# Kernel optimization log

Measured on AMD Instinct MI355X. Metric: run time of the kernel, lower is better.

The kernel has to match this reference:

```python
import jax, jax.numpy as jnp
import numpy as np

DIM = 512
L = 4096
B, H, W = 8, 64, 64
EPS = 1e-06
BN_EPS = 1e-05


def setup_inputs() -> dict:
    key = jax.random.key(0)
    ks = jax.random.split(key, 16)
    s = 1.0 / np.sqrt(DIM)
    d = {
        'x': jax.random.normal(ks[0], (B, DIM, H, W), dtype=jnp.float32),
        'pos_emb': jax.random.normal(ks[1], (1, L, DIM), dtype=jnp.float32),
        'Wq': jax.random.uniform(ks[2], (DIM, DIM), jnp.float32, -s, s),
        'bq': jax.random.uniform(ks[3], (DIM,), jnp.float32, -s, s),
        'Wk': jax.random.uniform(ks[4], (DIM, DIM), jnp.float32, -s, s),
        'bk': jax.random.uniform(ks[5], (DIM,), jnp.float32, -s, s),
        'Wv': jax.random.uniform(ks[6], (DIM, DIM), jnp.float32, -s, s),
        'bv': jax.random.uniform(ks[7], (DIM,), jnp.float32, -s, s),
        'Wq1': jax.random.uniform(ks[8], (DIM, DIM), jnp.float32, -s, s),
        'bq1': jax.random.uniform(ks[9], (DIM,), jnp.float32, -s, s),
        'Wk1': jax.random.uniform(ks[10], (DIM, DIM), jnp.float32, -s, s),
        'bk1': jax.random.uniform(ks[11], (DIM,), jnp.float32, -s, s),
        'gamma': jax.random.normal(ks[12], (1,), jnp.float32) * 0.1,
        'bn_weight': jnp.ones((DIM,), jnp.float32),
        'bn_bias': jnp.zeros((DIM,), jnp.float32),
    }
    return d


def reference(x, pos_emb, Wq, bq, Wk, bk, Wv, bv, Wq1, bq1, Wk1, bk1, gamma, bn_weight, bn_bias):
    Bb, C, Hh, Ww = x.shape
    # [B,C,H,W] -> [B, L, C] tokens
    xs = x.transpose(0, 2, 3, 1).reshape(Bb, Hh * Ww, C) + pos_emb
    Q = jax.nn.relu(xs @ Wq.T + bq)   # kernel_fun = ReLU
    K = jax.nn.relu(xs @ Wk.T + bk)
    V = xs @ Wv.T + bv
    Q1 = xs @ Wq1.T + bq1
    K1 = xs @ Wk1.T + bk1
    # torch einsum 'blc,bcc,bl->blc' uses only diag(KV); compute it directly:
    # diagKV[b,c] = sum_l K[b,l,c] * V[b,l,c]
    diagKV = jnp.einsum('blc,blc->bc', K, V)
    Ksum = K.sum(axis=1)  # == K^T summed over last axis, [B,C]
    Z = 1.0 / jnp.einsum('blc,bc->bl', Q, Ksum + EPS)
    result = Q * diagKV[:, None, :] * Z[:, :, None]  # [B,L,C]
    # channel-softmax attention: softmax over last dim of Q1^T @ K1, [B,C,C]
    mid = jax.nn.softmax(jnp.einsum('blc,bld->bcd', Q1, K1), axis=-1)
    result = result @ mid  # [B,L,C]
    xs = xs + gamma * result
    y = xs.transpose(0, 2, 1).reshape(Bb, C, Hh, Ww)
    # BatchNorm2d in training mode (fresh module): batch stats, biased variance
    mean = y.mean(axis=(0, 2, 3))
    var = y.var(axis=(0, 2, 3))
    yn = (y - mean[None, :, None, None]) * jax.lax.rsqrt(var + BN_EPS)[None, :, None, None]
    yn = yn * bn_weight[None, :, None, None] + bn_bias[None, :, None, None]
    return jax.nn.relu(yn)
```

## Files before the change

kernel.cpp:

```cpp
#include <hip/hip_runtime.h>
#include <stdint.h>

typedef float f32x4 __attribute__((ext_vector_type(4)));
typedef short bf16x8 __attribute__((ext_vector_type(8)));

__device__ __forceinline__ float bf2f(unsigned short h){
  union { unsigned int u; float f; } v; v.u = ((unsigned int)h) << 16; return v.f;
}
__device__ __forceinline__ unsigned short f2bf(float f){
  union { float f; unsigned int u; } v; v.f = f;
  return (unsigned short)((v.u + 0x7fffu + ((v.u >> 16) & 1u)) >> 16);
}

typedef __attribute__((address_space(1))) const unsigned int ga_u32;
typedef __attribute__((address_space(3))) unsigned int ls_u32;
__device__ __forceinline__ void async_load16(const void* g, void* l){
  __builtin_amdgcn_global_load_lds((ga_u32*)g, (ls_u32*)l, 16, 0, 0);
}

#define CFENCE() asm volatile("" ::: "memory")

__global__ __launch_bounds__(256) void k_prep_all(
    const float* __restrict__ w0, const float* __restrict__ w1,
    const float* __restrict__ w2, const float* __restrict__ w3,
    const float* __restrict__ w4,
    const float* __restrict__ b0, const float* __restrict__ b1,
    const float* __restrict__ b2, const float* __restrict__ b3,
    const float* __restrict__ b4,
    unsigned short* __restrict__ wbf, float* __restrict__ bias5,
    unsigned short* __restrict__ wq1x2)
{
  const int bid = blockIdx.x;
  const int t = threadIdx.x;
  if (bid < 5120){
    int slot = bid >> 10;
    int i = (bid & 1023) * 256 + t;
    const float* w = (slot == 0) ? w0 : (slot == 1) ? w1 :
                     (slot == 2) ? w2 : (slot == 3) ? w3 : w4;
    wbf[(size_t)slot * 262144 + i] = f2bf(w[i]);
  } else if (bid < 5130){
    int i = (bid - 5120) * 256 + t;
    int s = i >> 9, r = i & 511;
    const float* b = (s == 0) ? b0 : (s == 1) ? b1 : (s == 2) ? b2 :
                     (s == 3) ? b3 : b4;
    bias5[i] = b[r];
  } else {
    int e = bid - 5130;
    #pragma unroll
    for (int rep = 0; rep < 2; rep++){
      int idx = rep*256 + t;
      unsigned short v = f2bf(w3[e*512 + idx]);
      wq1x2[(size_t)e*1024 + idx] = v;
      wq1x2[(size_t)e*1024 + 512 + idx] = v;
    }
  }
}

__global__ __launch_bounds__(256) void k_build_xs(
    const float* __restrict__ x, const float* __restrict__ pos,
    unsigned short* __restrict__ xsb, unsigned short* __restrict__ xsT,
    float* __restrict__ svec)
{
  __shared__ float tile[64][65];
  __shared__ unsigned short tile2[64][72];
  __shared__ float sred[256];
  const int lt = blockIdx.x, ct = blockIdx.y;
  const int t = threadIdx.x;
  const int rr = t >> 3, c8 = (t & 7) * 8;
  float pr[16];
  #pragma unroll
  for (int pass = 0; pass < 2; pass++){
    int gl = lt*64 + rr + pass*32;
    f32x4 p0 = *(const f32x4*)(pos + (size_t)gl * 512 + ct*64 + c8);
    f32x4 p1 = *(const f32x4*)(pos + (size_t)gl * 512 + ct*64 + c8 + 4);
    #pragma unroll
    for (int s = 0; s < 4; s++){ pr[pass*8+s] = p0[s]; pr[pass*8+4+s] = p1[s]; }
  }
  for (int b = 0; b < 8; b++){
    #pragma unroll
    for (int pass = 0; pass < 2; pass++){
      int r = rr + pass * 32;
      const float* src = x + ((size_t)b * 512 + ct*64 + r) * 4096 + lt*64 + c8;
      f32x4 v0 = *(const f32x4*)src;
      f32x4 v1 = *(const f32x4*)(src + 4);
      #pragma unroll
      for (int s = 0; s < 4; s++){ tile[r][c8+s] = v0[s]; tile[r][c8+4+s] = v1[s]; }
    }
    __syncthreads();
    #pragma unroll
    for (int pass = 0; pass < 2; pass++){
      int ll = rr + pass * 32;
      int gl = lt*64 + ll;
      bf16x8 hv;
      #pragma unroll
      for (int s = 0; s < 8; s++){
        unsigned short h = f2bf(tile[c8+s][ll] + pr[pass*8+s]);
        hv[s] = (short)h;
        tile2[c8+s][ll] = h;
      }
      *(bf16x8*)(xsb + ((size_t)b * 4096 + gl) * 512 + ct*64 + c8) = hv;
    }
    __syncthreads();
    #pragma unroll
    for (int rep = 0; rep < 2; rep++){
      int c = rep*32 + (t >> 3);
      int l0 = (t & 7) * 8;
      bf16x8 v = *(const bf16x8*)&tile2[c][l0];
      *(bf16x8*)(xsT + ((size_t)b * 512 + ct*64 + c) * 4096 + lt*64 + l0) = v;
    }
    {
      const int c = t & 63, lq = t >> 6;
      float s_ = 0.f;
      #pragma unroll
      for (int j = 0; j < 16; j++) s_ += bf2f(tile2[c][lq*16 + j]);
      sred[t] = s_;
      __syncthreads();
      if (t < 64){
        float ss = sred[t] + sred[t+64] + sred[t+128] + sred[t+192];
        atomicAdd(&svec[b*512 + ct*64 + t], ss);
      }
    }
    __syncthreads();
  }
}

__global__ __launch_bounds__(64) void k_softmax(
    const float* __restrict__ S, unsigned short* __restrict__ mid)
{
  const size_t row = blockIdx.x;
  const int lane = threadIdx.x;
  const float* p = S + row * 512 + lane * 8;
  f32x4 v0 = *(const f32x4*)p, v1 = *(const f32x4*)(p + 4);
  float mx = v0[0];
  #pragma unroll
  for (int s = 1; s < 4; s++) mx = fmaxf(mx, v0[s]);
  #pragma unroll
  for (int s = 0; s < 4; s++) mx = fmaxf(mx, v1[s]);
  #pragma unroll
  for (int m = 1; m < 64; m <<= 1) mx = fmaxf(mx, __shfl_xor(mx, m));
  float e[8]; float sum = 0.f;
  #pragma unroll
  for (int s = 0; s < 4; s++){ e[s]   = __expf(v0[s] - mx); sum += e[s]; }
  #pragma unroll
  for (int s = 0; s < 4; s++){ e[4+s] = __expf(v1[s] - mx); sum += e[4+s]; }
  #pragma unroll
  for (int m = 1; m < 64; m <<= 1) sum += __shfl_xor(sum, m);
  float inv = 1.0f / sum;
  bf16x8 hv;
  #pragma unroll
  for (int s = 0; s < 8; s++) hv[s] = (short)f2bf(e[s] * inv);
  *(bf16x8*)(mid + row * 512 + lane * 8) = hv;
}

__global__ __launch_bounds__(256) void k_transpose_scale(
    const unsigned short* __restrict__ in, const float* __restrict__ diag,
    unsigned short* __restrict__ out)
{
  __shared__ float tile[64][65];
  const int rt = blockIdx.x, ct = blockIdx.y, z = blockIdx.z;
  const unsigned short* src = in  + (size_t)z * 262144;
  unsigned short*       dst = out + (size_t)z * 262144;
  const int t = threadIdx.x;
  const int rr = t >> 3, c8 = (t & 7) * 8;
  #pragma unroll
  for (int pass = 0; pass < 2; pass++){
    int r = rr + pass * 32;
    bf16x8 v = *(const bf16x8*)(src + (size_t)(rt*64 + r) * 512 + ct*64 + c8);
    #pragma unroll
    for (int s = 0; s < 8; s++) tile[r][c8+s] = bf2f((unsigned short)v[s]);
  }
  __syncthreads();
  f32x4 dg0 = *(const f32x4*)(diag + z*512 + rt*64 + c8);
  f32x4 dg1 = *(const f32x4*)(diag + z*512 + rt*64 + c8 + 4);
  #pragma unroll
  for (int pass = 0; pass < 2; pass++){
    int c = rr + pass * 32;
    bf16x8 hv;
    #pragma unroll
    for (int s = 0; s < 4; s++) hv[s]   = (short)f2bf(tile[c8+s][c]   * dg0[s]);
    #pragma unroll
    for (int s = 0; s < 4; s++) hv[4+s] = (short)f2bf(tile[c8+4+s][c] * dg1[s]);
    *(bf16x8*)(dst + (size_t)(ct*64 + c) * 512 + rt*64 + c8) = hv;
  }
}

#define GEMM_PRE()                                                            \
  const int tid = threadIdx.x;                                                \
  const int lane = tid & 63;                                                  \
  const int wave = tid >> 6;                                                  \
  const int wm = wave >> 1, wn = wave & 1;                                    \
  size_t aoff[4], boff[4]; int ldsq[4];                                       \
  _Pragma("unroll")                                                           \
  for (int i = 0; i < 4; i++){                                                \
    int qq = i*4 + wave;                                                      \
    int ch = qq*64 + lane;                                                    \
    int m  = ch >> 3, p = ch & 7;                                             \
    int lc = p ^ (m & 7);                                                     \
    aoff[i] = (size_t)(m0 + m) * K + lc*8;                                    \
    boff[i] = (size_t)m * K + lc*8;                                           \
    ldsq[i] = qq * 1024;                                                      \
  }                                                                           \
  f32x4 acc[4][4];                                                            \
  const f32x4 vzero = {0.f,0.f,0.f,0.f};                                      \
  _Pragma("unroll")                                                           \
  for (int i = 0; i < 4; i++)                                                 \
    _Pragma("unroll")                                                         \
    for (int j = 0; j < 4; j++) acc[i][j] = vzero;                            \
  int arow[4], brow[4];                                                       \
  _Pragma("unroll")                                                           \
  for (int f = 0; f < 4; f++){                                                \
    arow[f] = (wm*64 + f*16 + (lane & 15)) * 64;                              \
    brow[f] = (wn*64 + f*16 + (lane & 15)) * 64;                              \
  }                                                                           \
  const int kg = lane >> 4;                                                   \
  const int l7 = lane & 7;                                                    \
  const int l15 = lane & 15;

#define GEMM_STAGE2(buf, kt, BB)                                              \
  _Pragma("unroll")                                                           \
  for (int i = 0; i < 4; i++){                                                \
    async_load16(Ae + aoff[i] + (kt)*64, (char*)&smem[(buf)*8192] + ldsq[i]); \
    async_load16((BB) + boff[i] + (kt)*64, (char*)&smem[16384 + (buf)*8192] + ldsq[i]); \
  }

#define GEMM_COMPUTE2(buf, ACC)                                               \
  _Pragma("unroll")                                                           \
  for (int ks = 0; ks < 2; ks++){                                             \
    bf16x8 a[4], b[4];                                                        \
    const int pa = (ks*4 + kg) ^ l7;                                          \
    _Pragma("unroll")                                                         \
    for (int f = 0; f < 4; f++){                                              \
      a[f] = *(const bf16x8*)&smem[(buf)*8192 + arow[f] + pa*8];              \
      b[f] = *(const bf16x8*)&smem[16384 + (buf)*8192 + brow[f] + pa*8];      \
    }                                                                         \
    _Pragma("unroll")                                                         \
    for (int i = 0; i < 4; i++)                                               \
      _Pragma("unroll")                                                       \
      for (int j = 0; j < 4; j++)                                             \
        (ACC)[i][j] = __builtin_amdgcn_mfma_f32_16x16x32_bf16(a[i], b[j], (ACC)[i][j], 0, 0, 0); \
  }

#define GEMM_KLOOP2(nkt, BB)                                                  \
  GEMM_STAGE2(0, 0, BB);                                                      \
  __syncthreads();                                                            \
  { int cur = 0;                                                              \
    for (int kt = 0; kt < (nkt); kt++){                                       \
      if (kt + 1 < (nkt)) { GEMM_STAGE2(cur ^ 1, kt + 1, BB); }               \
      GEMM_COMPUTE2(cur, acc);                                                \
      __syncthreads();                                                        \
      cur ^= 1;                                                               \
    } }

__global__ __launch_bounds__(256, 2) void k_mega(
    const unsigned short* __restrict__ A,
    const unsigned short* __restrict__ xsT,
    const unsigned short* __restrict__ W,
    const float* __restrict__ bias5,
    const float* __restrict__ svec,
    unsigned short* __restrict__ Qb,
    unsigned short* __restrict__ Gstk,
    float* __restrict__ diag, float* __restrict__ ksum,
    float* __restrict__ uvec, float* __restrict__ wvec)
{
  __shared__ unsigned short smem[32768];
  const int bid = blockIdx.x;
  const int xcd = bid & 7, local = bid >> 3;

  if (local < 32){
    const int gw = xcd*32 + local;
    const int part = gw & 1;
    const int ntile = (gw >> 1) & 3;
    const int mtile = (gw >> 3) & 3;
    const int z = gw >> 5;
    const int m0 = mtile * 128, n0 = ntile * 128;
    const int K = 4096;
    const unsigned short* Ae = xsT + (size_t)z * 2097152 + part * 2048;
    const unsigned short* Be = Ae + (size_t)n0 * 4096;

    GEMM_PRE();
    GEMM_KLOOP2(32, Be);

    #pragma unroll
    for (int j = 0; j < 4; j++){
      const int cl = wn*64 + j*16 + l15;
      #pragma unroll
      for (int i = 0; i < 4; i++){
        const int rb = wm*64 + i*16 + kg*4;
        #pragma unroll
        for (int q = 0; q < 4; q++)
          smem[(rb + q)*136 + cl] = f2bf(acc[i][j][q]);
      }
    }
    __syncthreads();
    #pragma unroll
    for (int rep = 0; rep < 8; rep++){
      const int rl = rep*16 + (tid >> 4);
      const int c0 = (tid & 15) * 8;
      bf16x8 v = *(const bf16x8*)&smem[rl*136 + c0];
      *(bf16x8*)(Gstk + (size_t)z*524288 + (size_t)(m0 + rl)*1024 + part*512 + n0 + c0) = v;
    }
    return;
  }

  if (local >= 288){
    const int uwid = xcd*2 + (local - 288);
    const int sel = uwid & 1, b = uwid >> 1;
    const int t = threadIdx.x;
    float* sv = (float*)(void*)smem;
    sv[t] = svec[b*512 + t]; sv[t+256] = svec[b*512 + t + 256];
    __syncthreads();
    const unsigned short* Wp = W + (size_t)(3 + sel) * 262144;
    float* o = sel ? wvec : uvec;
    #pragma unroll
    for (int rep = 0; rep < 2; rep++){
      int e = rep*256 + t;
      const unsigned short* row = Wp + (size_t)e * 512;
      float acc_ = 0.f;
      for (int ch = 0; ch < 64; ch++){
        bf16x8 v = *(const bf16x8*)(row + ch*8);
        #pragma unroll
        for (int j = 0; j < 8; j++) acc_ += bf2f((unsigned short)v[j]) * sv[ch*8+j];
      }
      o[b*512 + e] = acc_;
    }
    return;
  }

  const int pw = xcd*256 + (local - 32);
  const int mtile = pw >> 3;
  const int unit  = pw & 7;
  const int m0 = mtile * 128;
  const int K = 512;
  const unsigned short* Ae = A;

  int mode, cb;
  const unsigned short* BeK; const unsigned short* BeV = W;
  if (unit < 4){ mode = 0; cb = unit*128;     BeK = W + (size_t)cb * 512; }
  else         { mode = 1; cb = (unit-4)*128; BeK = W + 262144 + (size_t)cb * 512;
                                              BeV = W + 524288 + (size_t)cb * 512; }

  GEMM_PRE();

  if (mode == 1){
    const int bz = mtile >> 5;
    GEMM_STAGE2(0, 0, BeK);
    __syncthreads();
    int cur = 0;
    for (int kt = 0; kt < 8; kt++){
      if (kt < 7) { GEMM_STAGE2(cur ^ 1, kt + 1, BeK); }
      else        { GEMM_STAGE2(cur ^ 1, 0, BeV); }
      GEMM_COMPUTE2(cur, acc);
      __syncthreads();
      cur ^= 1;
    }
    GEMM_STAGE2(cur ^ 1, 1, BeV);
    unsigned int kpk[4][4][2];
    #pragma unroll
    for (int j = 0; j < 4; j++){
      const int cj = cb + wn*64 + j*16 + l15;
      const float bb = bias5[512 + cj];
      float ks_ = 0.f;
      #pragma unroll
      for (int i = 0; i < 4; i++){
        #pragma unroll
        for (int h = 0; h < 2; h++){
          float v0 = acc[i][j][2*h]   + bb; v0 = v0 > 0.f ? v0 : 0.f;
          float v1 = acc[i][j][2*h+1] + bb; v1 = v1 > 0.f ? v1 : 0.f;
          unsigned short h0 = f2bf(v0), h1 = f2bf(v1);
          kpk[i][j][h] = (unsigned)h0 | ((unsigned)h1 << 16);
          ks_ += bf2f(h0) + bf2f(h1);
        }
        acc[i][j] = vzero;
      }
      ks_ += __shfl_xor(ks_, 16);
      ks_ += __shfl_xor(ks_, 32);
      if (lane < 16) atomicAdd(&ksum[bz*512 + cj], ks_);
    }
    for (int kt = 0; kt < 8; kt++){
      if (kt >= 1 && kt < 7) { GEMM_STAGE2(cur ^ 1, kt + 1, BeV); }
      GEMM_COMPUTE2(cur, acc);
      __syncthreads();
      cur ^= 1;
    }
    #pragma unroll
    for (int j = 0; j < 4; j++){
      const int cj = cb + wn*64 + j*16 + l15;
      const float bb = bias5[1024 + cj];
      float dv = 0.f;
      #pragma unroll
      for (int i = 0; i < 4; i++){
        #pragma unroll
        for (int h = 0; h < 2; h++){
          float v0 = bf2f(f2bf(acc[i][j][2*h]   + bb));
          float v1 = bf2f(f2bf(acc[i][j][2*h+1] + bb));
          dv += bf2f((unsigned short)(kpk[i][j][h] & 0xffffu)) * v0
              + bf2f((unsigned short)(kpk[i][j][h] >> 16))     * v1;
        }
      }
      dv += __shfl_xor(dv, 16);
      dv += __shfl_xor(dv, 32);
      if (lane < 16) atomicAdd(&diag[bz*512 + cj], dv);
    }
    return;
  }

  GEMM_KLOOP2(8, BeK);

  #pragma unroll
  for (int j = 0; j < 4; j++){
    const int cl = wn*64 + j*16 + l15;
    const float bb = bias5[cb + cl];
    #pragma unroll
    for (int i = 0; i < 4; i++){
      const int rb = wm*64 + i*16 + kg*4;
      #pragma unroll
      for (int q = 0; q < 4; q++){
        float v = acc[i][j][q] + bb; v = v > 0.f ? v : 0.f;
        smem[(rb + q)*136 + cl] = f2bf(v);
      }
    }
  }
  __syncthreads();
  #pragma unroll
  for (int rep = 0; rep < 8; rep++){
    const int rl = rep*16 + (tid >> 4);
    const int c0 = (tid & 15) * 8;
    bf16x8 v = *(const bf16x8*)&smem[rl*136 + c0];
    *(bf16x8*)(Qb + (size_t)(m0 + rl) * 512 + cb + c0) = v;
  }
}

__global__ __launch_bounds__(256) void k_pz(
    const unsigned short* __restrict__ Wq1x2,
    const unsigned short* __restrict__ Gstk,
    unsigned short* __restrict__ P,
    const unsigned short* __restrict__ Qb,
    const float* __restrict__ ksum,
    float* __restrict__ Z)
{
  __shared__ unsigned short smem[32768];
  const int bid = blockIdx.x;

  if (bid >= 128){
    const int row = (bid - 128) * 4 + ((int)threadIdx.x >> 6);
    const int lane = threadIdx.x & 63;
    const int b = row >> 12;
    bf16x8 q = *(const bf16x8*)(Qb + (size_t)row * 512 + lane * 8);
    f32x4 k0 = *(const f32x4*)(ksum + b*512 + lane*8);
    f32x4 k1 = *(const f32x4*)(ksum + b*512 + lane*8 + 4);
    float den = 0.f;
    #pragma unroll
    for (int s = 0; s < 4; s++) den += bf2f((unsigned short)q[s])   * (k0[s] + 1e-6f);
    #pragma unroll
    for (int s = 0; s < 4; s++) den += bf2f((unsigned short)q[4+s]) * (k1[s] + 1e-6f);
    #pragma unroll
    for (int m = 1; m < 64; m <<= 1) den += __shfl_xor(den, m);
    if (lane == 0) Z[row] = 1.0f / den;
    return;
  }

  const int wgid = (bid & 7) * 16 + (bid >> 3);
  const int z = wgid >> 4;
  const int mtile = (wgid >> 2) & 3, ntile = wgid & 3;
  const int m0 = mtile * 128, n0 = ntile * 128;
  const int K = 1024;
  const unsigned short* Ae = Wq1x2;
  const unsigned short* Be = Gstk + (size_t)z * 524288 + (size_t)n0 * 1024;

  GEMM_PRE();
  GEMM_KLOOP2(16, Be);

  #pragma unroll
  for (int j = 0; j < 4; j++){
    const int cl = wn*64 + j*16 + l15;
    #pragma unroll
    for (int i = 0; i < 4; i++){
      const int rb = wm*64 + i*16 + kg*4;
      #pragma unroll
      for (int q = 0; q < 4; q++)
        smem[(rb + q)*136 + cl] = f2bf(acc[i][j][q]);
    }
  }
  __syncthreads();
  #pragma unroll
  for (int rep = 0; rep < 8; rep++){
    const int rl = rep*16 + (tid >> 4);
    const int c0 = (tid & 15) * 8;
    bf16x8 v = *(const bf16x8*)&smem[rl*136 + c0];
    *(bf16x8*)(P + (size_t)z * 262144 + (size_t)(m0 + rl) * 512 + n0 + c0) = v;
  }
}

__global__ __launch_bounds__(256) void gemm_S(
    const unsigned short* __restrict__ P,
    const unsigned short* __restrict__ Wk1b,
    const float* __restrict__ bias5,
    const float* __restrict__ u, const float* __restrict__ w,
    float* __restrict__ Sf)
{
  __shared__ unsigned short smem[32768];
  const int bid = blockIdx.x;
  const int wgid = (bid & 7) * 16 + (bid >> 3);
  const int z = wgid >> 4;
  const int mtile = (wgid >> 2) & 3, ntile = wgid & 3;
  const int m0 = mtile * 128, n0 = ntile * 128;
  const int K = 512;
  const unsigned short* Ae = P + (size_t)z * 262144;
  const unsigned short* Be = Wk1b + (size_t)n0 * 512;

  GEMM_PRE();
  GEMM_KLOOP2(8, Be);

  #pragma unroll
  for (int j = 0; j < 4; j++){
    int cd = n0 + wn*64 + j*16 + l15;
    float bkv = bias5[2048 + cd];
    float wv  = w[z*512 + cd] + 4096.0f * bkv;
    #pragma unroll
    for (int i = 0; i < 4; i++){
      int r = m0 + wm*64 + i*16 + kg*4;
      #pragma unroll
      for (int q = 0; q < 4; q++){
        int rr = r + q;
        float uq  = u[z*512 + rr];
        float bqv = bias5[1536 + rr];
        Sf[(size_t)z * 262144 + (size_t)rr * 512 + cd] =
            acc[i][j][q] + uq * bkv + bqv * wv;
      }
    }
  }
}

__global__ __launch_bounds__(256, 2) void gemm_res2(
    const unsigned short* __restrict__ A,
    const unsigned short* __restrict__ Bt,
    const float* __restrict__ Zp,
    unsigned short* __restrict__ outh,
    const float* __restrict__ gamma_p,
    float* __restrict__ bnS, float* __restrict__ bnQ)
{
  __shared__ unsigned short smem[32768];
  __shared__ float zbuf[128];
  const int bid = blockIdx.x;
  const int wgid = (bid & 7) * 128 + (bid >> 3);
  const int mtile = wgid >> 2;
  const int ntile = wgid & 3;
  const int m0 = mtile * 128;
  const int nc0 = ntile * 128;
  const int K = 512;
  const unsigned short* Ae = A;
  const unsigned short* Be =
      Bt + (size_t)(mtile >> 5) * 262144 + (size_t)nc0 * 512;

  GEMM_PRE();
  GEMM_KLOOP2(8, Be);

  const float g = gamma_p[0];
  if (tid < 128) zbuf[tid] = Zp[m0 + tid];
  __syncthreads();
  #pragma unroll
  for (int j = 0; j < 4; j++){
    const int cl = wn*64 + j*16 + l15;
    #pragma unroll
    for (int i = 0; i < 4; i++){
      const int rb = wm*64 + i*16 + kg*4;
      #pragma unroll
      for (int q = 0; q < 4; q++){
        const int rl = rb + q;
        smem[rl*136 + cl] = f2bf(g * zbuf[rl] * acc[i][j][q]);
      }
    }
  }
  __syncthreads();
  float sc[8] = {0.f,0.f,0.f,0.f,0.f,0.f,0.f,0.f};
  float sq[8] = {0.f,0.f,0.f,0.f,0.f,0.f,0.f,0.f};
  const int c0 = (tid & 15) * 8;
  #pragma unroll
  for (int rep = 0; rep < 8; rep++){
    const int rl = rep*16 + (tid >> 4);
    bf16x8 ga = *(const bf16x8*)&smem[rl*136 + c0];
    size_t gidx = (size_t)(m0 + rl) * 512 + nc0 + c0;
    bf16x8 xv = *(const bf16x8*)(outh + gidx);
    bf16x8 yv;
    #pragma unroll
    for (int j = 0; j < 8; j++){
      float y = bf2f((unsigned short)xv[j]) + bf2f((unsigned short)ga[j]);
      yv[j] = (short)f2bf(y);
      sc[j] += y; sq[j] += y * y;
    }
    *(bf16x8*)(outh + gidx) = yv;
  }
  __syncthreads();
  float* red = (float*)(void*)smem;
  const int tg = tid >> 4;
  f32x4 s0 = {sc[0],sc[1],sc[2],sc[3]}, s1 = {sc[4],sc[5],sc[6],sc[7]};
  f32x4 q0 = {sq[0],sq[1],sq[2],sq[3]}, q1 = {sq[4],sq[5],sq[6],sq[7]};
  *(f32x4*)&red[tg*128 + c0]        = s0;  *(f32x4*)&red[tg*128 + c0 + 4]        = s1;
  *(f32x4*)&red[2048 + tg*128 + c0] = q0;  *(f32x4*)&red[2048 + tg*128 + c0 + 4] = q1;
  __syncthreads();
  if (tid < 128){
    float ss = 0.f, qq = 0.f;
    #pragma unroll
    for (int gg = 0; gg < 16; gg++){
      ss += red[gg*128 + tid];
      qq += red[2048 + gg*128 + tid];
    }
    atomicAdd(&bnS[nc0 + tid], ss);
    atomicAdd(&bnQ[nc0 + tid], qq);
  }
}

__global__ __launch_bounds__(256) void k_bn_finalize(
    const unsigned short* __restrict__ y, const float* __restrict__ bnS,
    const float* __restrict__ bnQ, const float* __restrict__ bnw,
    const float* __restrict__ bnb, float* __restrict__ out)
{
  __shared__ float tile[64][65];
  __shared__ float scale_s[64], shift_s[64];
  const int lt = blockIdx.x, ct = blockIdx.y, b = blockIdx.z;
  const int t = threadIdx.x;
  if (t < 64){
    int c = ct*64 + t;
    float s = bnS[c], q = bnQ[c];
    float mean = s * (1.0f / 32768.0f);
    float var  = q * (1.0f / 32768.0f) - mean * mean;
    float inv  = rsqrtf(var + 1e-5f);
    float scv  = bnw[c] * inv;
    scale_s[t] = scv;
    shift_s[t] = bnb[c] - mean * scv;
  }
  const int rr = t >> 3, c8 = (t & 7) * 8;
  #pragma unroll
  for (int pass = 0; pass < 2; pass++){
    int l = rr + pass * 32;
    bf16x8 v = *(const bf16x8*)(y + ((size_t)b * 4096 + lt*64 + l) * 512 + ct*64 + c8);
    #pragma unroll
    for (int s = 0; s < 8; s++) tile[l][c8+s] = bf2f((unsigned short)v[s]);
  }
  __syncthreads();
  #pragma unroll
  for (int pass = 0; pass < 2; pass++){
    int c = rr + pass * 32;
    float scv = scale_s[c], sh = shift_s[c];
    f32x4 o0, o1;
    #pragma unroll
    for (int s = 0; s < 4; s++){
      float v = tile[c8+s][c] * scv + sh;     o0[s] = v > 0.f ? v : 0.f;
      float w = tile[c8+4+s][c] * scv + sh;   o1[s] = w > 0.f ? w : 0.f;
    }
    float* dp = out + ((size_t)b * 512 + ct*64 + c) * 4096 + lt*64 + c8;
    *(f32x4*)dp = o0;
    *(f32x4*)(dp + 4) = o1;
  }
}

extern "C" void kernel_launch(void* const* d_in, const int* in_sizes, int n_in,
                              void* d_out, int out_size, void* d_ws, size_t ws_size,
                              hipStream_t stream)
{
  const float* x    = (const float*)d_in[0];
  const float* pos  = (const float*)d_in[1];
  const float* Wq   = (const float*)d_in[2];
  const float* bq   = (const float*)d_in[3];
  const float* Wk   = (const float*)d_in[4];
  const float* bk   = (const float*)d_in[5];
  const float* Wv   = (const float*)d_in[6];
  const float* bv   = (const float*)d_in[7];
  const float* Wq1  = (const float*)d_in[8];
  const float* bq1  = (const float*)d_in[9];
  const float* Wk1  = (const float*)d_in[10];
  const float* bk1  = (const float*)d_in[11];
  const float* gam  = (const float*)d_in[12];
  const float* bnw  = (const float*)d_in[13];
  const float* bnb  = (const float*)d_in[14];
  float* out = (float*)d_out;
  char* ws = (char*)d_ws;

  const size_t MB = 1ull << 20;
  const size_t OFF_XSB  = 0;
  const size_t OFF_QB   = 32*MB;
  const size_t OFF_XST  = 64*MB;
  const size_t OFF_GSTK = 96*MB;
  const size_t OFF_PBF  = 104*MB;
  const size_t OFF_SF   = 108*MB;
  const size_t OFF_MIDB = 116*MB;
  const size_t OFF_MIDT = 120*MB;
  const size_t OFF_WBF  = 124*MB;
  const size_t OFF_WQ2  = 127*MB;
  const size_t OFF_B5   = 128*MB + 512*1024;
  const size_t OFF_UV   = 129*MB;
  const size_t OFF_WV   = OFF_UV + 16384;
  const size_t OFF_Z    = OFF_WV + 16384;
  const size_t OFF_DIAG = 130*MB;
  const size_t OFF_KSUM = OFF_DIAG + 16384;
  const size_t OFF_BNS  = OFF_KSUM + 16384;
  const size_t OFF_BNQ  = OFF_BNS + 2048;
  const size_t OFF_SV   = OFF_BNQ + 2048;
  const size_t ZERO_LEN = 16384 + 16384 + 2048 + 2048 + 16384;
  const size_t WS_NEED  = OFF_SV + 16384;
  if (ws_size < WS_NEED) return;

  unsigned short* xsb  = (unsigned short*)(ws + OFF_XSB);
  unsigned short* Qb   = (unsigned short*)(ws + OFF_QB);
  unsigned short* xsT  = (unsigned short*)(ws + OFF_XST);
  unsigned short* Gstk = (unsigned short*)(ws + OFF_GSTK);
  unsigned short* Pbf  = (unsigned short*)(ws + OFF_PBF);
  float*          Sf   = (float*)(ws + OFF_SF);
  unsigned short* midb = (unsigned short*)(ws + OFF_MIDB);
  unsigned short* midT = (unsigned short*)(ws + OFF_MIDT);
  unsigned short* wbf  = (unsigned short*)(ws + OFF_WBF);
  unsigned short* wq1x2= (unsigned short*)(ws + OFF_WQ2);
  float* bias5 = (float*)(ws + OFF_B5);
  float* uvec = (float*)(ws + OFF_UV);
  float* wvec = (float*)(ws + OFF_WV);
  float* Zp   = (float*)(ws + OFF_Z);
  float* diag = (float*)(ws + OFF_DIAG);
  float* ksum = (float*)(ws + OFF_KSUM);
  float* bnS  = (float*)(ws + OFF_BNS);
  float* bnQ  = (float*)(ws + OFF_BNQ);
  float* svec = (float*)(ws + OFF_SV);

  hipMemsetAsync(ws + OFF_DIAG, 0, ZERO_LEN, stream);

  k_prep_all<<<dim3(5642), 256, 0, stream>>>(Wq, Wk, Wv, Wq1, Wk1,
                                             bq, bk, bv, bq1, bk1,
                                             wbf, bias5, wq1x2);

  k_build_xs<<<dim3(64, 8), 256, 0, stream>>>(x, pos, xsb, xsT, svec);

  k_mega<<<dim3(2320), 256, 0, stream>>>(xsb, xsT, wbf, bias5, svec,
                                         Qb, Gstk, diag, ksum, uvec, wvec);

  k_pz<<<dim3(8320), 256, 0, stream>>>(wq1x2, Gstk, Pbf, Qb, ksum, Zp);

  gemm_S<<<dim3(128), 256, 0, stream>>>(Pbf, wbf + 4*262144, bias5, uvec, wvec, Sf);

  k_softmax<<<dim3(4096), 64, 0, stream>>>(Sf, midb);
  k_transpose_scale<<<dim3(8, 8, 8), 256, 0, stream>>>(midb, diag, midT);

  gemm_res2<<<dim3(1024), 256, 0, stream>>>(Qb, midT, Zp, xsb, gam, bnS, bnQ);

  k_bn_finalize<<<dim3(64, 8, 8), 256, 0, stream>>>(xsb, bnS, bnQ, bnw, bnb, out);
}
```

Before: 220.4 us.

## Merge weight prep with xs build and fuse softmax with scaled transpose

Result: faster. 215.6 us (-2.2%).

```diff
diff --git a/kernel.cpp b/kernel.cpp
--- a/kernel.cpp
+++ b/kernel.cpp
@@ -20,52 +20,53 @@
 
 #define CFENCE() asm volatile("" ::: "memory")
 
-__global__ __launch_bounds__(256) void k_prep_all(
+__global__ __launch_bounds__(256) void k_prep_build(
+    const float* __restrict__ x, const float* __restrict__ pos,
     const float* __restrict__ w0, const float* __restrict__ w1,
     const float* __restrict__ w2, const float* __restrict__ w3,
     const float* __restrict__ w4,
     const float* __restrict__ b0, const float* __restrict__ b1,
     const float* __restrict__ b2, const float* __restrict__ b3,
     const float* __restrict__ b4,
+    unsigned short* __restrict__ xsb, unsigned short* __restrict__ xsT,
+    float* __restrict__ svec,
     unsigned short* __restrict__ wbf, float* __restrict__ bias5,
     unsigned short* __restrict__ wq1x2)
-{
-  const int bid = blockIdx.x;
-  const int t = threadIdx.x;
-  if (bid < 5120){
-    int slot = bid >> 10;
-    int i = (bid & 1023) * 256 + t;
-    const float* w = (slot == 0) ? w0 : (slot == 1) ? w1 :
-                     (slot == 2) ? w2 : (slot == 3) ? w3 : w4;
-    wbf[(size_t)slot * 262144 + i] = f2bf(w[i]);
-  } else if (bid < 5130){
-    int i = (bid - 5120) * 256 + t;
-    int s = i >> 9, r = i & 511;
-    const float* b = (s == 0) ? b0 : (s == 1) ? b1 : (s == 2) ? b2 :
-                     (s == 3) ? b3 : b4;
-    bias5[i] = b[r];
-  } else {
-    int e = bid - 5130;
-    #pragma unroll
-    for (int rep = 0; rep < 2; rep++){
-      int idx = rep*256 + t;
-      unsigned short v = f2bf(w3[e*512 + idx]);
-      wq1x2[(size_t)e*1024 + idx] = v;
-      wq1x2[(size_t)e*1024 + 512 + idx] = v;
-    }
-  }
-}
-
-__global__ __launch_bounds__(256) void k_build_xs(
-    const float* __restrict__ x, const float* __restrict__ pos,
-    unsigned short* __restrict__ xsb, unsigned short* __restrict__ xsT,
-    float* __restrict__ svec)
 {
   __shared__ float tile[64][65];
   __shared__ unsigned short tile2[64][72];
   __shared__ float sred[256];
-  const int lt = blockIdx.x, ct = blockIdx.y;
+  const int bid = blockIdx.x;
   const int t = threadIdx.x;
+
+  if (bid >= 512){
+    if (bid < 5632){
+      int wbid = bid - 512;
+      int slot = wbid >> 10;
+      int i = (wbid & 1023) * 256 + t;
+      const float* w = (slot == 0) ? w0 : (slot == 1) ? w1 :
+                       (slot == 2) ? w2 : (slot == 3) ? w3 : w4;
+      wbf[(size_t)slot * 262144 + i] = f2bf(w[i]);
+    } else if (bid < 5642){
+      int i = (bid - 5632) * 256 + t;
+      int s = i >> 9, r = i & 511;
+      const float* b = (s == 0) ? b0 : (s == 1) ? b1 : (s == 2) ? b2 :
+                       (s == 3) ? b3 : b4;
+      bias5[i] = b[r];
+    } else {
+      int e = bid - 5642;
+      #pragma unroll
+      for (int rep = 0; rep < 2; rep++){
+        int idx = rep*256 + t;
+        unsigned short v = f2bf(w3[e*512 + idx]);
+        wq1x2[(size_t)e*1024 + idx] = v;
+        wq1x2[(size_t)e*1024 + 512 + idx] = v;
+      }
+    }
+    return;
+  }
+
+  const int lt = bid & 63, ct = bid >> 6;
   const int rr = t >> 3, c8 = (t & 7) * 8;
   float pr[16];
   #pragma unroll
@@ -124,63 +125,46 @@
   }
 }
 
-__global__ __launch_bounds__(64) void k_softmax(
-    const float* __restrict__ S, unsigned short* __restrict__ mid)
+__global__ __launch_bounds__(256) void k_softmax_t2(
+    const float* __restrict__ Sf, const float* __restrict__ diag,
+    unsigned short* __restrict__ midT)
 {
-  const size_t row = blockIdx.x;
-  const int lane = threadIdx.x;
-  const float* p = S + row * 512 + lane * 8;
-  f32x4 v0 = *(const f32x4*)p, v1 = *(const f32x4*)(p + 4);
-  float mx = v0[0];
-  #pragma unroll
-  for (int s = 1; s < 4; s++) mx = fmaxf(mx, v0[s]);
-  #pragma unroll
-  for (int s = 0; s < 4; s++) mx = fmaxf(mx, v1[s]);
-  #pragma unroll
-  for (int m = 1; m < 64; m <<= 1) mx = fmaxf(mx, __shfl_xor(mx, m));
-  float e[8]; float sum = 0.f;
-  #pragma unroll
-  for (int s = 0; s < 4; s++){ e[s]   = __expf(v0[s] - mx); sum += e[s]; }
-  #pragma unroll
-  for (int s = 0; s < 4; s++){ e[4+s] = __expf(v1[s] - mx); sum += e[4+s]; }
-  #pragma unroll
-  for (int m = 1; m < 64; m <<= 1) sum += __shfl_xor(sum, m);
-  float inv = 1.0f / sum;
-  bf16x8 hv;
-  #pragma unroll
-  for (int s = 0; s < 8; s++) hv[s] = (short)f2bf(e[s] * inv);
-  *(bf16x8*)(mid + row * 512 + lane * 8) = hv;
-}
-
-__global__ __launch_bounds__(256) void k_transpose_scale(
-    const unsigned short* __restrict__ in, const float* __restrict__ diag,
-    unsigned short* __restrict__ out)
-{
-  __shared__ float tile[64][65];
-  const int rt = blockIdx.x, ct = blockIdx.y, z = blockIdx.z;
-  const unsigned short* src = in  + (size_t)z * 262144;
-  unsigned short*       dst = out + (size_t)z * 262144;
+  __shared__ unsigned short tr[8][520];
+  const int rc = blockIdx.x, z = blockIdx.y;
   const int t = threadIdx.x;
-  const int rr = t >> 3, c8 = (t & 7) * 8;
-  #pragma unroll
-  for (int pass = 0; pass < 2; pass++){
-    int r = rr + pass * 32;
-    bf16x8 v = *(const bf16x8*)(src + (size_t)(rt*64 + r) * 512 + ct*64 + c8);
-    #pragma unroll
-    for (int s = 0; s < 8; s++) tile[r][c8+s] = bf2f((unsigned short)v[s]);
+  const int w = t >> 6, lane = t & 63;
+  #pragma unroll
+  for (int rr = 0; rr < 2; rr++){
+    int cl = w*2 + rr;
+    int c = rc*8 + cl;
+    const float* p = Sf + ((size_t)z*512 + c)*512 + lane*8;
+    f32x4 v0 = *(const f32x4*)p, v1 = *(const f32x4*)(p + 4);
+    float mx = v0[0];
+    #pragma unroll
+    for (int s = 1; s < 4; s++) mx = fmaxf(mx, v0[s]);
+    #pragma unroll
+    for (int s = 0; s < 4; s++) mx = fmaxf(mx, v1[s]);
+    #pragma unroll
+    for (int m = 1; m < 64; m <<= 1) mx = fmaxf(mx, __shfl_xor(mx, m));
+    float e[8]; float sum = 0.f;
+    #pragma unroll
+    for (int s = 0; s < 4; s++){ e[s]   = __expf(v0[s] - mx); sum += e[s]; }
+    #pragma unroll
+    for (int s = 0; s < 4; s++){ e[4+s] = __expf(v1[s] - mx); sum += e[4+s]; }
+    #pragma unroll
+    for (int m = 1; m < 64; m <<= 1) sum += __shfl_xor(sum, m);
+    float scl = diag[z*512 + c] / sum;
+    #pragma unroll
+    for (int s = 0; s < 8; s++) tr[cl][lane*8 + s] = f2bf(e[s] * scl);
   }
   __syncthreads();
-  f32x4 dg0 = *(const f32x4*)(diag + z*512 + rt*64 + c8);
-  f32x4 dg1 = *(const f32x4*)(diag + z*512 + rt*64 + c8 + 4);
-  #pragma unroll
-  for (int pass = 0; pass < 2; pass++){
-    int c = rr + pass * 32;
+  #pragma unroll
+  for (int rep = 0; rep < 2; rep++){
+    int d = rep*256 + t;
     bf16x8 hv;
     #pragma unroll
-    for (int s = 0; s < 4; s++) hv[s]   = (short)f2bf(tile[c8+s][c]   * dg0[s]);
-    #pragma unroll
-    for (int s = 0; s < 4; s++) hv[4+s] = (short)f2bf(tile[c8+4+s][c] * dg1[s]);
-    *(bf16x8*)(dst + (size_t)(ct*64 + c) * 512 + rt*64 + c8) = hv;
+    for (int s = 0; s < 8; s++) hv[s] = (short)tr[s][d];
+    *(bf16x8*)(midT + ((size_t)z*512 + d)*512 + rc*8) = hv;
   }
 }
 
@@ -683,7 +667,6 @@
   const size_t OFF_GSTK = 96*MB;
   const size_t OFF_PBF  = 104*MB;
   const size_t OFF_SF   = 108*MB;
-  const size_t OFF_MIDB = 116*MB;
   const size_t OFF_MIDT = 120*MB;
   const size_t OFF_WBF  = 124*MB;
   const size_t OFF_WQ2  = 127*MB;
@@ -706,7 +689,6 @@
   unsigned short* Gstk = (unsigned short*)(ws + OFF_GSTK);
   unsigned short* Pbf  = (unsigned short*)(ws + OFF_PBF);
   float*          Sf   = (float*)(ws + OFF_SF);
-  unsigned short* midb = (unsigned short*)(ws + OFF_MIDB);
   unsigned short* midT = (unsigned short*)(ws + OFF_MIDT);
   unsigned short* wbf  = (unsigned short*)(ws + OFF_WBF);
   unsigned short* wq1x2= (unsigned short*)(ws + OFF_WQ2);
@@ -722,11 +704,9 @@
 
   hipMemsetAsync(ws + OFF_DIAG, 0, ZERO_LEN, stream);
 
-  k_prep_all<<<dim3(5642), 256, 0, stream>>>(Wq, Wk, Wv, Wq1, Wk1,
-                                             bq, bk, bv, bq1, bk1,
-                                             wbf, bias5, wq1x2);
-
-  k_build_xs<<<dim3(64, 8), 256, 0, stream>>>(x, pos, xsb, xsT, svec);
+  k_prep_build<<<dim3(6154), 256, 0, stream>>>(
+      x, pos, Wq, Wk, Wv, Wq1, Wk1, bq, bk, bv, bq1, bk1,
+      xsb, xsT, svec, wbf, bias5, wq1x2);
 
   k_mega<<<dim3(2320), 256, 0, stream>>>(xsb, xsT, wbf, bias5, svec,
                                          Qb, Gstk, diag, ksum, uvec, wvec);
@@ -735,8 +715,7 @@
 
   gemm_S<<<dim3(128), 256, 0, stream>>>(Pbf, wbf + 4*262144, bias5, uvec, wvec, Sf);
 
-  k_softmax<<<dim3(4096), 64, 0, stream>>>(Sf, midb);
-  k_transpose_scale<<<dim3(8, 8, 8), 256, 0, stream>>>(midb, diag, midT);
+  k_softmax_t2<<<dim3(64, 8), 256, 0, stream>>>(Sf, diag, midT);
 
   gemm_res2<<<dim3(1024), 256, 0, stream>>>(Qb, midT, Zp, xsb, gam, bnS, bnQ);
 
```
